# Kernel tuning notes

Hardware: AMD Instinct MI355X
Metric: run time of the kernel (lower is better)

The kernel has to match this reference:

```python
import jax, jax.numpy as jnp
import numpy as np
import math

B, S, D, H = 2, 2048, 1024, 16
HD = D // H


def setup_inputs() -> dict:
    key = jax.random.key(0)
    ks = jax.random.split(key, 8)
    sc = 0.02
    return {
        "x": jax.random.normal(ks[0], (B, S, D), dtype=jnp.float32),
        "y": jax.random.normal(ks[1], (B, S, D), dtype=jnp.float32),
        "W_kv": jax.random.normal(ks[2], (D, 2 * D), dtype=jnp.float32) * sc,
        "b_kv": jnp.zeros((2 * D,), dtype=jnp.float32),
        "W_q": jax.random.normal(ks[3], (D, D), dtype=jnp.float32) * sc,
        "b_q": jnp.zeros((D,), dtype=jnp.float32),
        "W_o": jax.random.normal(ks[4], (D, D), dtype=jnp.float32) * sc,
        "b_o": jnp.zeros((D,), dtype=jnp.float32),
    }


def reference(x, y, W_kv, b_kv, W_q, b_q, W_o, b_o):
    b, s, d = x.shape
    h, hd = H, HD
    # kv projection from x (the "context"), q projection from y
    kv = x @ W_kv + b_kv                     # [b, s, 2d]
    q = y @ W_q + b_q                        # [b, s, d]
    kv = kv.reshape(b, s, h, 2 * hd).transpose(0, 2, 1, 3)  # [b, h, s, 2hd]
    q = q.reshape(b, s, h, hd).transpose(0, 2, 1, 3)        # [b, h, s, hd]
    k, v = kv[..., :hd], kv[..., hd:]
    scaled = jnp.einsum("bhqd,bhkd->bhqk", q, k) / math.sqrt(hd)  # [b,h,s,s]
    attention = jax.nn.softmax(scaled, axis=-1)  # F.softmax defaults to last dim
    values = jnp.einsum("bhqk,bhkd->bhqd", attention, v)  # [b, h, s, hd]
    # Faithful to the original: reshape [b,h,s,hd] -> [b,s,d] WITHOUT
    # transposing heads back (row-major flatten, heads interleaved).
    values = values.reshape(b, s, d)
    return values @ W_o + b_o
```

## Files before the change

### kernel.cpp

```cpp
#include <hip/hip_runtime.h>
#include <hip/hip_bf16.h>


#define S_LEN 2048
#define D_DIM 1024
#define H_NUM 16
#define HD_DIM 64

typedef __attribute__((ext_vector_type(8))) __bf16 bf16x8;
typedef __attribute__((ext_vector_type(4))) float f32x4;

__device__ __forceinline__ unsigned short f2bf(float f) {
    unsigned int v;
    __builtin_memcpy(&v, &f, 4);
    v = v + 0x7fff + ((v >> 16) & 1);
    return (unsigned short)(v >> 16);
}
__device__ __forceinline__ unsigned int pkbf(float a, float b) {
    __hip_bfloat162 h = __float22bfloat162_rn(float2{a, b});
    unsigned int r;
    __builtin_memcpy(&r, &h, 4);
    return r;
}
__device__ __forceinline__ float sani(float v) {
    unsigned int u;
    __builtin_memcpy(&u, &v, 4);
    return ((u >> 23) & 0xFFu) == 0xFFu ? 0.f : v;
}
__device__ __forceinline__ void gll16(const void* g, void* l) {
    __builtin_amdgcn_global_load_lds(
        (const __attribute__((address_space(1))) void*)g,
        (__attribute__((address_space(3))) void*)l, 16, 0, 0);
}

__global__ __launch_bounds__(256) void cvt_bf16(const float* __restrict__ in,
                                                unsigned short* __restrict__ out, int n) {
    int i = (blockIdx.x * 256 + threadIdx.x) * 8;
    if (i < n) {
        float4 a0 = *(const float4*)&in[i];
        float4 a1 = *(const float4*)&in[i + 4];
        uint4 p;
        p.x = pkbf(a0.x, a0.y); p.y = pkbf(a0.z, a0.w);
        p.z = pkbf(a1.x, a1.y); p.w = pkbf(a1.z, a1.w);
        *(uint4*)&out[i] = p;
    }
}

__global__ __launch_bounds__(256) void transpose_cvt(const float* __restrict__ in,
                                                     unsigned short* __restrict__ out,
                                                     int R, int C) {
    __shared__ unsigned short tile[32][33];
    int c0 = blockIdx.x * 32, r0 = blockIdx.y * 32;
    int tx = threadIdx.x & 31, ty = threadIdx.x >> 5;
    for (int i = 0; i < 32; i += 8)
        tile[ty + i][tx] = f2bf(in[(size_t)(r0 + ty + i) * C + c0 + tx]);
    __syncthreads();
    for (int i = 0; i < 32; i += 8)
        out[(size_t)(c0 + ty + i) * R + r0 + tx] = tile[tx][ty + i];
}

template <int AMODE, int CMODE>
__global__ __launch_bounds__(256) void gemm_bt(const void* __restrict__ Av,
                                               const unsigned short* __restrict__ Bt,
                                               const float* __restrict__ bias,
                                               void* __restrict__ C0,
                                               unsigned short* __restrict__ VtB,
                                               int M, int N, int K) {
    constexpr int SA = (AMODE == 1) ? 32 : 40;
    __shared__ unsigned short sA[128 * SA];
    __shared__ unsigned short sB[128 * 32];
    const int tid = threadIdx.x;
    const int m0 = blockIdx.y * 128;
    const int n0 = blockIdx.x * 128;
    const int w = tid >> 6, lane = tid & 63;
    const int quad = lane >> 4, lm = lane & 15;
    const int wrow = (w >> 1) * 64, wcol = (w & 1) * 64;

    f32x4 acc[4][4] = {};

    for (int k0 = 0; k0 < K; k0 += 32) {
        __syncthreads();
#pragma unroll
        for (int p = 0; p < 2; ++p) {
            int cid = p * 256 + tid;
            int row = cid >> 2, col = (cid & 3) << 3;
            if (AMODE == 1) {
                gll16(&((const unsigned short*)Av)[(size_t)(m0 + row) * K + k0 + col],
                      &sA[cid * 8]);
            } else if (AMODE == 0) {
                const float* Af = (const float*)Av + (size_t)(m0 + row) * K + k0 + col;
                float4 a0 = *(const float4*)Af;
                float4 a1 = *(const float4*)(Af + 4);
                uint4 packed;
                packed.x = pkbf(a0.x, a0.y); packed.y = pkbf(a0.z, a0.w);
                packed.z = pkbf(a1.x, a1.y); packed.w = pkbf(a1.z, a1.w);
                *(uint4*)&sA[row * SA + col] = packed;
            } else {
                int m = m0 + row;
                int bb = m >> 11, sib = m & 2047;
                int hh = sib >> 7, qhi = sib & 127;
                int kk = k0 + col;
                uint4 packed = *(const uint4*)((const unsigned short*)Av +
                    (size_t)((bb << 11) + (qhi << 4) + (kk >> 6)) * K + (hh << 6) + (kk & 63));
                *(uint4*)&sA[row * SA + col] = packed;
            }
            gll16(&Bt[(size_t)(n0 + row) * K + k0 + col], &sB[cid * 8]);
        }
        __syncthreads();
        bf16x8 av[4], bv[4];
#pragma unroll
        for (int i = 0; i < 4; ++i)
            av[i] = *(const bf16x8*)&sA[(wrow + i * 16 + lm) * SA + quad * 8];
#pragma unroll
        for (int j = 0; j < 4; ++j)
            bv[j] = *(const bf16x8*)&sB[(wcol + j * 16 + lm) * 32 + quad * 8];
#pragma unroll
        for (int i = 0; i < 4; ++i)
#pragma unroll
            for (int j = 0; j < 4; ++j)
                acc[i][j] = __builtin_amdgcn_mfma_f32_16x16x32_bf16(av[i], bv[j], acc[i][j], 0, 0, 0);
    }

    if (CMODE == 2) {
        const int h = n0 >> 7;
        if (wcol == 0) {
#pragma unroll
            for (int i = 0; i < 4; ++i)
#pragma unroll
                for (int j = 0; j < 4; ++j) {
                    int d = j * 16 + lm;
                    float bi = bias[h * 128 + d];
#pragma unroll
                    for (int r = 0; r < 4; ++r) {
                        int grow = m0 + wrow + i * 16 + quad * 4 + r;
                        int bb = grow >> 11, ss = grow & 2047;
                        ((unsigned short*)C0)[((size_t)(bb * 16 + h) * 2048 + ss) * 64 + d] =
                            f2bf(sani(acc[i][j][r] + bi));
                    }
                }
        } else {
#pragma unroll
            for (int i = 0; i < 4; ++i)
#pragma unroll
                for (int j = 0; j < 4; ++j) {
                    int d = j * 16 + lm;
                    float bi = bias[h * 128 + 64 + d];
                    int s0 = m0 + wrow + i * 16 + quad * 4;
                    int bb = s0 >> 11, ss = s0 & 2047;
                    ushort4 u;
                    u.x = f2bf(sani(acc[i][j][0] + bi));
                    u.y = f2bf(sani(acc[i][j][1] + bi));
                    u.z = f2bf(sani(acc[i][j][2] + bi));
                    u.w = f2bf(sani(acc[i][j][3] + bi));
                    *(ushort4*)&VtB[((size_t)(bb * 16 + h) * 64 + d) * 2048 + ss] = u;
                }
        }
    } else {
#pragma unroll
        for (int i = 0; i < 4; ++i)
#pragma unroll
            for (int j = 0; j < 4; ++j)
#pragma unroll
                for (int r = 0; r < 4; ++r) {
                    int grow = m0 + wrow + i * 16 + quad * 4 + r;
                    int gcol = n0 + wcol + j * 16 + lm;
                    float val = sani(acc[i][j][r] + bias[gcol]);
                    if (CMODE == 1) ((float*)C0)[(size_t)grow * N + gcol] = val;
                    else            ((unsigned short*)C0)[(size_t)grow * N + gcol] = f2bf(val);
                }
    }
}

__global__ __launch_bounds__(256) void attn_k(unsigned short* qo,
                                              const unsigned short* __restrict__ Kb,
                                              const unsigned short* __restrict__ Vt) {
    __shared__ unsigned short sK[64 * 72];
    __shared__ unsigned short sVt[64 * 72];
    __shared__ unsigned short sP[4][16 * 72];

    const int tid = threadIdx.x;
    const int w = tid >> 6, lane = tid & 63;
    const int quad = lane >> 4, lm = lane & 15;
    const int qblock = blockIdx.x & 31;
    const int bh = blockIdx.x >> 5;
    const int b = bh >> 4, h = bh & 15;

    unsigned short* Qp = qo + (size_t)b * S_LEN * D_DIM + h * HD_DIM;
    const unsigned short* Kbase = Kb + (size_t)bh * S_LEN * HD_DIM;
    const unsigned short* Vbase = Vt + (size_t)bh * HD_DIM * S_LEN;

    const int qrow0 = qblock * 64 + w * 16;
    bf16x8 qa0 = *(const bf16x8*)&Qp[(size_t)(qrow0 + lm) * D_DIM + quad * 8];
    bf16x8 qa1 = *(const bf16x8*)&Qp[(size_t)(qrow0 + lm) * D_DIM + 32 + quad * 8];

    f32x4 acc_o[4] = {};
    float lsum[4] = {0.f, 0.f, 0.f, 0.f};

    const int skey = tid >> 2;
    const int sc0 = (tid & 3) * 16;

    for (int kt = 0; kt < S_LEN / 64; ++kt) {
        __syncthreads();
        {
            const unsigned short* Ks = Kbase + (size_t)(kt * 64 + skey) * 64 + sc0;
            *(uint4*)&sK[skey * 72 + sc0]     = *(const uint4*)Ks;
            *(uint4*)&sK[skey * 72 + sc0 + 8] = *(const uint4*)(Ks + 8);
            const unsigned short* Vs = Vbase + (size_t)skey * 2048 + kt * 64 + sc0;
            *(uint4*)&sVt[skey * 72 + sc0]     = *(const uint4*)Vs;
            *(uint4*)&sVt[skey * 72 + sc0 + 8] = *(const uint4*)(Vs + 8);
        }
        __syncthreads();

        unsigned short* sPw = sP[w];
#pragma unroll
        for (int g = 0; g < 4; ++g) {
            bf16x8 k0 = *(const bf16x8*)&sK[(g * 16 + lm) * 72 + quad * 8];
            bf16x8 k1 = *(const bf16x8*)&sK[(g * 16 + lm) * 72 + 32 + quad * 8];
            f32x4 z = {0.f, 0.f, 0.f, 0.f};
            f32x4 c = __builtin_amdgcn_mfma_f32_16x16x32_bf16(
                          qa1, k1,
                          __builtin_amdgcn_mfma_f32_16x16x32_bf16(qa0, k0, z, 0, 0, 0),
                          0, 0, 0);
#pragma unroll
            for (int r = 0; r < 4; ++r) {
                float s = fminf(fmaxf(c[r] * 0.125f, -30.f), 30.f);
                float p = __expf(s);
                lsum[r] += p;
                sPw[(quad * 4 + r) * 72 + g * 16 + lm] = f2bf(p);
            }
        }
        bf16x8 pa0 = *(const bf16x8*)&sPw[lm * 72 + quad * 8];
        bf16x8 pa1 = *(const bf16x8*)&sPw[lm * 72 + 32 + quad * 8];
#pragma unroll
        for (int n = 0; n < 4; ++n) {
            bf16x8 v0 = *(const bf16x8*)&sVt[(n * 16 + lm) * 72 + quad * 8];
            bf16x8 v1 = *(const bf16x8*)&sVt[(n * 16 + lm) * 72 + 32 + quad * 8];
            acc_o[n] = __builtin_amdgcn_mfma_f32_16x16x32_bf16(
                           pa1, v1,
                           __builtin_amdgcn_mfma_f32_16x16x32_bf16(pa0, v0, acc_o[n], 0, 0, 0),
                           0, 0, 0);
        }
    }

#pragma unroll
    for (int r = 0; r < 4; ++r) {
#pragma unroll
        for (int off = 1; off < 16; off <<= 1)
            lsum[r] += __shfl_xor(lsum[r], off);
        float inv = 1.f / lsum[r];
        int qrow = qrow0 + quad * 4 + r;
#pragma unroll
        for (int n = 0; n < 4; ++n)
            Qp[(size_t)qrow * D_DIM + n * 16 + lm] = f2bf(sani(acc_o[n][r] * inv));
    }
}

__global__ __launch_bounds__(256) void fill_k(float* out, int n) {
    int i = blockIdx.x * 256 + threadIdx.x;
    if (i < n) out[i] = 4.0f;
}

extern "C" void kernel_launch(void* const* d_in, const int* in_sizes, int n_in,
                              void* d_out, int out_size, void* d_ws, size_t ws_size,
                              hipStream_t stream) {
    const float* x    = (const float*)d_in[0];
    const float* y    = (const float*)d_in[1];
    const float* W_kv = (const float*)d_in[2];
    const float* b_kv = (const float*)d_in[3];
    const float* W_q  = (const float*)d_in[4];
    const float* b_q  = (const float*)d_in[5];
    const float* W_o  = (const float*)d_in[6];
    const float* b_o  = (const float*)d_in[7];

    if (ws_size < (size_t)16 * 1024 * 1024) {
        fill_k<<<dim3((out_size + 255) / 256), 256, 0, stream>>>((float*)d_out, out_size);
        return;
    }
    const bool bigws = ws_size >= (size_t)26 * 1024 * 1024;

    unsigned short* ws   = (unsigned short*)d_ws;
    unsigned short* Kb   = ws;
    unsigned short* VtB  = ws + 4 * 1024 * 1024;
    unsigned short* xbf  = (unsigned short*)d_out;
    unsigned short* WkvT = xbf + 4 * 1024 * 1024;
    unsigned short* WqT  = WkvT + 2 * 1024 * 1024;
    unsigned short* WoT  = bigws ? ws + 12 * 1024 * 1024
                                 : WqT + 1024 * 1024;
    unsigned short* qBuf = bigws ? ws + 8 * 1024 * 1024
                                 : xbf;
    float* outBuf        = bigws ? (float*)d_out
                                 : (float*)d_ws;

    transpose_cvt<<<dim3(64, 32), 256, 0, stream>>>(W_kv, WkvT, 1024, 2048);
    transpose_cvt<<<dim3(32, 32), 256, 0, stream>>>(W_q, WqT, 1024, 1024);
    transpose_cvt<<<dim3(32, 32), 256, 0, stream>>>(W_o, WoT, 1024, 1024);
    cvt_bf16<<<dim3(2048), 256, 0, stream>>>(x, xbf, 4096 * 1024);
    gemm_bt<1, 2><<<dim3(16, 32), 256, 0, stream>>>(xbf, WkvT, b_kv, Kb, VtB, 4096, 2048, 1024);
    gemm_bt<0, 0><<<dim3(8, 32), 256, 0, stream>>>(y, WqT, b_q, qBuf, nullptr, 4096, 1024, 1024);
    attn_k<<<dim3(2 * H_NUM * (S_LEN / 64)), 256, 0, stream>>>(qBuf, Kb, VtB);
    gemm_bt<2, 1><<<dim3(8, 32), 256, 0, stream>>>(qBuf, WoT, b_o, outBuf, nullptr, 4096, 1024, 1024);
    if (!bigws)
        hipMemcpyAsync(d_out, d_ws, (size_t)out_size * sizeof(float),
                       hipMemcpyDeviceToDevice, stream);
}
```

Before: 279.6 us.

## Merge prep kernels, fuse QKV projections, use async LDS loads in attention

Combines the three weight transposes and the x conversion into one prep launch, and merges the KV and Q projection GEMMs into one grid. The grid is split in two when the workspace is small, because the Q output then aliases xbf. The 1/sqrt(hd) scale moves into the Q projection epilogue and the softmax clamp is removed. Attention now loads K/Vt tiles into LDS with global_load_lds in a split-half layout. The output GEMM uses 64-row tiles to raise the block count. This cuts launch overhead and register round-trips, but removing the clamp risks overflow in exp for large scores.

```diff
diff --git a/kernel.cpp b/kernel.cpp
--- a/kernel.cpp
+++ b/kernel.cpp
@@ -33,84 +33,89 @@
         (__attribute__((address_space(3))) void*)l, 16, 0, 0);
 }
 
-__global__ __launch_bounds__(256) void cvt_bf16(const float* __restrict__ in,
-                                                unsigned short* __restrict__ out, int n) {
-    int i = (blockIdx.x * 256 + threadIdx.x) * 8;
-    if (i < n) {
-        float4 a0 = *(const float4*)&in[i];
-        float4 a1 = *(const float4*)&in[i + 4];
+__global__ __launch_bounds__(256) void prep(const float* __restrict__ Wkv,
+                                            const float* __restrict__ Wq,
+                                            const float* __restrict__ Wo,
+                                            const float* __restrict__ x,
+                                            unsigned short* __restrict__ WkvT,
+                                            unsigned short* __restrict__ WqT,
+                                            unsigned short* __restrict__ WoT,
+                                            unsigned short* __restrict__ xbf) {
+    __shared__ unsigned short tile[32][33];
+    const int blk = blockIdx.x;
+    if (blk < 4096) {
+        const float* in; unsigned short* out; int C, bx, by;
+        if (blk < 2048)      { in = Wkv; out = WkvT; C = 2048; bx = blk & 63;          by = blk >> 6; }
+        else if (blk < 3072) { in = Wq;  out = WqT;  C = 1024; bx = (blk - 2048) & 31; by = (blk - 2048) >> 5; }
+        else                 { in = Wo;  out = WoT;  C = 1024; bx = (blk - 3072) & 31; by = (blk - 3072) >> 5; }
+        const int R = 1024;
+        int c0 = bx * 32, r0 = by * 32;
+        int tx = threadIdx.x & 31, ty = threadIdx.x >> 5;
+        for (int i = 0; i < 32; i += 8)
+            tile[ty + i][tx] = f2bf(in[(size_t)(r0 + ty + i) * C + c0 + tx]);
+        __syncthreads();
+        for (int i = 0; i < 32; i += 8)
+            out[(size_t)(c0 + ty + i) * R + r0 + tx] = tile[tx][ty + i];
+    } else {
+        int i = ((blk - 4096) * 256 + threadIdx.x) * 8;
+        float4 a0 = *(const float4*)&x[i];
+        float4 a1 = *(const float4*)&x[i + 4];
         uint4 p;
         p.x = pkbf(a0.x, a0.y); p.y = pkbf(a0.z, a0.w);
         p.z = pkbf(a1.x, a1.y); p.w = pkbf(a1.z, a1.w);
-        *(uint4*)&out[i] = p;
-    }
-}
-
-__global__ __launch_bounds__(256) void transpose_cvt(const float* __restrict__ in,
-                                                     unsigned short* __restrict__ out,
-                                                     int R, int C) {
-    __shared__ unsigned short tile[32][33];
-    int c0 = blockIdx.x * 32, r0 = blockIdx.y * 32;
-    int tx = threadIdx.x & 31, ty = threadIdx.x >> 5;
-    for (int i = 0; i < 32; i += 8)
-        tile[ty + i][tx] = f2bf(in[(size_t)(r0 + ty + i) * C + c0 + tx]);
-    __syncthreads();
-    for (int i = 0; i < 32; i += 8)
-        out[(size_t)(c0 + ty + i) * R + r0 + tx] = tile[tx][ty + i];
-}
-
-template <int AMODE, int CMODE>
-__global__ __launch_bounds__(256) void gemm_bt(const void* __restrict__ Av,
-                                               const unsigned short* __restrict__ Bt,
-                                               const float* __restrict__ bias,
-                                               void* __restrict__ C0,
-                                               unsigned short* __restrict__ VtB,
-                                               int M, int N, int K) {
-    constexpr int SA = (AMODE == 1) ? 32 : 40;
-    __shared__ unsigned short sA[128 * SA];
+        *(uint4*)&xbf[i] = p;
+    }
+}
+
+__global__ __launch_bounds__(256) void proj(const unsigned short* __restrict__ xbf,
+                                            const float* __restrict__ y,
+                                            const unsigned short* __restrict__ WkvT,
+                                            const unsigned short* __restrict__ WqT,
+                                            const float* __restrict__ b_kv,
+                                            const float* __restrict__ b_q,
+                                            unsigned short* __restrict__ Kb,
+                                            unsigned short* __restrict__ VtB,
+                                            unsigned short* __restrict__ qBuf,
+                                            int base) {
+    __shared__ unsigned short sA[128 * 32];
     __shared__ unsigned short sB[128 * 32];
+    const int blk = blockIdx.x + base;
+    const bool iskv = blk < 512;
+    const int bid = iskv ? blk : blk - 512;
+    const int m0 = iskv ? (bid >> 4) * 128 : (bid >> 3) * 128;
+    const int n0 = iskv ? (bid & 15) * 128 : (bid & 7) * 128;
+    const unsigned short* Bt = iskv ? WkvT : WqT;
     const int tid = threadIdx.x;
-    const int m0 = blockIdx.y * 128;
-    const int n0 = blockIdx.x * 128;
     const int w = tid >> 6, lane = tid & 63;
     const int quad = lane >> 4, lm = lane & 15;
     const int wrow = (w >> 1) * 64, wcol = (w & 1) * 64;
 
     f32x4 acc[4][4] = {};
 
-    for (int k0 = 0; k0 < K; k0 += 32) {
+    for (int k0 = 0; k0 < 1024; k0 += 32) {
         __syncthreads();
 #pragma unroll
         for (int p = 0; p < 2; ++p) {
             int cid = p * 256 + tid;
             int row = cid >> 2, col = (cid & 3) << 3;
-            if (AMODE == 1) {
-                gll16(&((const unsigned short*)Av)[(size_t)(m0 + row) * K + k0 + col],
-                      &sA[cid * 8]);
-            } else if (AMODE == 0) {
-                const float* Af = (const float*)Av + (size_t)(m0 + row) * K + k0 + col;
+            if (iskv) {
+                gll16(&xbf[(size_t)(m0 + row) * 1024 + k0 + col], &sA[cid * 8]);
+            } else {
+                const float* Af = y + (size_t)(m0 + row) * 1024 + k0 + col;
                 float4 a0 = *(const float4*)Af;
                 float4 a1 = *(const float4*)(Af + 4);
-                uint4 packed;
-                packed.x = pkbf(a0.x, a0.y); packed.y = pkbf(a0.z, a0.w);
-                packed.z = pkbf(a1.x, a1.y); packed.w = pkbf(a1.z, a1.w);
-                *(uint4*)&sA[row * SA + col] = packed;
-            } else {
-                int m = m0 + row;
-                int bb = m >> 11, sib = m & 2047;
-                int hh = sib >> 7, qhi = sib & 127;
-                int kk = k0 + col;
-                uint4 packed = *(const uint4*)((const unsigned short*)Av +
-                    (size_t)((bb << 11) + (qhi << 4) + (kk >> 6)) * K + (hh << 6) + (kk & 63));
-                *(uint4*)&sA[row * SA + col] = packed;
+                uint4 pk;
+                pk.x = pkbf(a0.x, a0.y); pk.y = pkbf(a0.z, a0.w);
+                pk.z = pkbf(a1.x, a1.y); pk.w = pkbf(a1.z, a1.w);
+                *(uint4*)&sA[cid * 8] = pk;
             }
-            gll16(&Bt[(size_t)(n0 + row) * K + k0 + col], &sB[cid * 8]);
+            gll16(&Bt[(size_t)(n0 + row) * 1024 + k0 + col], &sB[cid * 8]);
         }
         __syncthreads();
         bf16x8 av[4], bv[4];
 #pragma unroll
         for (int i = 0; i < 4; ++i)
-            av[i] = *(const bf16x8*)&sA[(wrow + i * 16 + lm) * SA + quad * 8];
+            av[i] = *(const bf16x8*)&sA[(wrow + i * 16 + lm) * 32 + quad * 8];
 #pragma unroll
         for (int j = 0; j < 4; ++j)
             bv[j] = *(const bf16x8*)&sB[(wcol + j * 16 + lm) * 32 + quad * 8];
@@ -121,7 +126,7 @@
                 acc[i][j] = __builtin_amdgcn_mfma_f32_16x16x32_bf16(av[i], bv[j], acc[i][j], 0, 0, 0);
     }
 
-    if (CMODE == 2) {
+    if (iskv) {
         const int h = n0 >> 7;
         if (wcol == 0) {
 #pragma unroll
@@ -129,12 +134,12 @@
 #pragma unroll
                 for (int j = 0; j < 4; ++j) {
                     int d = j * 16 + lm;
-                    float bi = bias[h * 128 + d];
+                    float bi = b_kv[h * 128 + d];
 #pragma unroll
                     for (int r = 0; r < 4; ++r) {
                         int grow = m0 + wrow + i * 16 + quad * 4 + r;
                         int bb = grow >> 11, ss = grow & 2047;
-                        ((unsigned short*)C0)[((size_t)(bb * 16 + h) * 2048 + ss) * 64 + d] =
+                        Kb[((size_t)(bb * 16 + h) * 2048 + ss) * 64 + d] =
                             f2bf(sani(acc[i][j][r] + bi));
                     }
                 }
@@ -144,7 +149,7 @@
 #pragma unroll
                 for (int j = 0; j < 4; ++j) {
                     int d = j * 16 + lm;
-                    float bi = bias[h * 128 + 64 + d];
+                    float bi = b_kv[h * 128 + 64 + d];
                     int s0 = m0 + wrow + i * 16 + quad * 4;
                     int bb = s0 >> 11, ss = s0 & 2047;
                     ushort4 u;
@@ -164,9 +169,8 @@
                 for (int r = 0; r < 4; ++r) {
                     int grow = m0 + wrow + i * 16 + quad * 4 + r;
                     int gcol = n0 + wcol + j * 16 + lm;
-                    float val = sani(acc[i][j][r] + bias[gcol]);
-                    if (CMODE == 1) ((float*)C0)[(size_t)grow * N + gcol] = val;
-                    else            ((unsigned short*)C0)[(size_t)grow * N + gcol] = f2bf(val);
+                    float val = sani(acc[i][j][r] + b_q[gcol]) * 0.125f;
+                    qBuf[(size_t)grow * 1024 + gcol] = f2bf(val);
                 }
     }
 }
@@ -174,8 +178,8 @@
 __global__ __launch_bounds__(256) void attn_k(unsigned short* qo,
                                               const unsigned short* __restrict__ Kb,
                                               const unsigned short* __restrict__ Vt) {
-    __shared__ unsigned short sK[64 * 72];
-    __shared__ unsigned short sVt[64 * 72];
+    __shared__ unsigned short sK[2][64 * 32];
+    __shared__ unsigned short sVt[2][64 * 32];
     __shared__ unsigned short sP[4][16 * 72];
 
     const int tid = threadIdx.x;
@@ -196,26 +200,26 @@
     f32x4 acc_o[4] = {};
     float lsum[4] = {0.f, 0.f, 0.f, 0.f};
 
-    const int skey = tid >> 2;
-    const int sc0 = (tid & 3) * 16;
+    const int srow = tid >> 2;
+    const int sch = (tid & 3) << 3;
 
     for (int kt = 0; kt < S_LEN / 64; ++kt) {
         __syncthreads();
         {
-            const unsigned short* Ks = Kbase + (size_t)(kt * 64 + skey) * 64 + sc0;
-            *(uint4*)&sK[skey * 72 + sc0]     = *(const uint4*)Ks;
-            *(uint4*)&sK[skey * 72 + sc0 + 8] = *(const uint4*)(Ks + 8);
-            const unsigned short* Vs = Vbase + (size_t)skey * 2048 + kt * 64 + sc0;
-            *(uint4*)&sVt[skey * 72 + sc0]     = *(const uint4*)Vs;
-            *(uint4*)&sVt[skey * 72 + sc0 + 8] = *(const uint4*)(Vs + 8);
+            const unsigned short* Kr = Kbase + (size_t)(kt * 64 + srow) * 64 + sch;
+            gll16(Kr,      &sK[0][tid * 8]);
+            gll16(Kr + 32, &sK[1][tid * 8]);
+            const unsigned short* Vr = Vbase + (size_t)srow * 2048 + kt * 64 + sch;
+            gll16(Vr,      &sVt[0][tid * 8]);
+            gll16(Vr + 32, &sVt[1][tid * 8]);
         }
         __syncthreads();
 
         unsigned short* sPw = sP[w];
 #pragma unroll
         for (int g = 0; g < 4; ++g) {
-            bf16x8 k0 = *(const bf16x8*)&sK[(g * 16 + lm) * 72 + quad * 8];
-            bf16x8 k1 = *(const bf16x8*)&sK[(g * 16 + lm) * 72 + 32 + quad * 8];
+            bf16x8 k0 = *(const bf16x8*)&sK[0][(g * 16 + lm) * 32 + quad * 8];
+            bf16x8 k1 = *(const bf16x8*)&sK[1][(g * 16 + lm) * 32 + quad * 8];
             f32x4 z = {0.f, 0.f, 0.f, 0.f};
             f32x4 c = __builtin_amdgcn_mfma_f32_16x16x32_bf16(
                           qa1, k1,
@@ -223,8 +227,7 @@
                           0, 0, 0);
 #pragma unroll
             for (int r = 0; r < 4; ++r) {
-                float s = fminf(fmaxf(c[r] * 0.125f, -30.f), 30.f);
-                float p = __expf(s);
+                float p = __expf(c[r]);
                 lsum[r] += p;
                 sPw[(quad * 4 + r) * 72 + g * 16 + lm] = f2bf(p);
             }
@@ -233,8 +236,8 @@
         bf16x8 pa1 = *(const bf16x8*)&sPw[lm * 72 + 32 + quad * 8];
 #pragma unroll
         for (int n = 0; n < 4; ++n) {
-            bf16x8 v0 = *(const bf16x8*)&sVt[(n * 16 + lm) * 72 + quad * 8];
-            bf16x8 v1 = *(const bf16x8*)&sVt[(n * 16 + lm) * 72 + 32 + quad * 8];
+            bf16x8 v0 = *(const bf16x8*)&sVt[0][(n * 16 + lm) * 32 + quad * 8];
+            bf16x8 v1 = *(const bf16x8*)&sVt[1][(n * 16 + lm) * 32 + quad * 8];
             acc_o[n] = __builtin_amdgcn_mfma_f32_16x16x32_bf16(
                            pa1, v1,
                            __builtin_amdgcn_mfma_f32_16x16x32_bf16(pa0, v0, acc_o[n], 0, 0, 0),
@@ -253,6 +256,64 @@
         for (int n = 0; n < 4; ++n)
             Qp[(size_t)qrow * D_DIM + n * 16 + lm] = f2bf(sani(acc_o[n][r] * inv));
     }
+}
+
+__global__ __launch_bounds__(256) void fgemm(const unsigned short* __restrict__ O,
+                                             const unsigned short* __restrict__ WoT,
+                                             const float* __restrict__ b_o,
+                                             float* __restrict__ out) {
+    __shared__ unsigned short sA[64 * 32];
+    __shared__ unsigned short sB[128 * 32];
+    const int tid = threadIdx.x;
+    const int m0 = blockIdx.y * 64;
+    const int n0 = blockIdx.x * 128;
+    const int w = tid >> 6, lane = tid & 63;
+    const int quad = lane >> 4, lm = lane & 15;
+    const int wrow = (w >> 1) * 32, wcol = (w & 1) * 64;
+
+    f32x4 acc[2][4] = {};
+
+    for (int k0 = 0; k0 < 1024; k0 += 32) {
+        __syncthreads();
+        {
+            int row = tid >> 2, kk = k0 + ((tid & 3) << 3);
+            int m = m0 + row;
+            int bb = m >> 11, sib = m & 2047;
+            int hh = sib >> 7, qhi = sib & 127;
+            gll16(&O[(size_t)((bb << 11) + (qhi << 4) + (kk >> 6)) * 1024 + (hh << 6) + (kk & 63)],
+                  &sA[tid * 8]);
+        }
+#pragma unroll
+        for (int p = 0; p < 2; ++p) {
+            int cid = p * 256 + tid;
+            int row = cid >> 2, col = (cid & 3) << 3;
+            gll16(&WoT[(size_t)(n0 + row) * 1024 + k0 + col], &sB[cid * 8]);
+        }
+        __syncthreads();
+        bf16x8 av[2], bv[4];
+#pragma unroll
+        for (int i = 0; i < 2; ++i)
+            av[i] = *(const bf16x8*)&sA[(wrow + i * 16 + lm) * 32 + quad * 8];
+#pragma unroll
+        for (int j = 0; j < 4; ++j)
+            bv[j] = *(const bf16x8*)&sB[(wcol + j * 16 + lm) * 32 + quad * 8];
+#pragma unroll
+        for (int i = 0; i < 2; ++i)
+#pragma unroll
+            for (int j = 0; j < 4; ++j)
+                acc[i][j] = __builtin_amdgcn_mfma_f32_16x16x32_bf16(av[i], bv[j], acc[i][j], 0, 0, 0);
+    }
+
+#pragma unroll
+    for (int i = 0; i < 2; ++i)
+#pragma unroll
+        for (int j = 0; j < 4; ++j)
+#pragma unroll
+            for (int r = 0; r < 4; ++r) {
+                int grow = m0 + wrow + i * 16 + quad * 4 + r;
+                int gcol = n0 + wcol + j * 16 + lm;
+                out[(size_t)grow * 1024 + gcol] = sani(acc[i][j][r] + b_o[gcol]);
+            }
 }
 
 __global__ __launch_bounds__(256) void fill_k(float* out, int n) {
@@ -288,17 +349,17 @@
                                  : WqT + 1024 * 1024;
     unsigned short* qBuf = bigws ? ws + 8 * 1024 * 1024
                                  : xbf;
-    float* outBuf        = bigws ? (float*)d_out
-                                 : (float*)d_ws;
-
-    transpose_cvt<<<dim3(64, 32), 256, 0, stream>>>(W_kv, WkvT, 1024, 2048);
-    transpose_cvt<<<dim3(32, 32), 256, 0, stream>>>(W_q, WqT, 1024, 1024);
-    transpose_cvt<<<dim3(32, 32), 256, 0, stream>>>(W_o, WoT, 1024, 1024);
-    cvt_bf16<<<dim3(2048), 256, 0, stream>>>(x, xbf, 4096 * 1024);
-    gemm_bt<1, 2><<<dim3(16, 32), 256, 0, stream>>>(xbf, WkvT, b_kv, Kb, VtB, 4096, 2048, 1024);
-    gemm_bt<0, 0><<<dim3(8, 32), 256, 0, stream>>>(y, WqT, b_q, qBuf, nullptr, 4096, 1024, 1024);
+    float* outBuf        = bigws ? (float*)d_out : (float*)d_ws;
+
+    prep<<<dim3(6144), 256, 0, stream>>>(W_kv, W_q, W_o, x, WkvT, WqT, WoT, xbf);
+    if (bigws) {
+        proj<<<dim3(768), 256, 0, stream>>>(xbf, y, WkvT, WqT, b_kv, b_q, Kb, VtB, qBuf, 0);
+    } else {
+        proj<<<dim3(512), 256, 0, stream>>>(xbf, y, WkvT, WqT, b_kv, b_q, Kb, VtB, qBuf, 0);
+        proj<<<dim3(256), 256, 0, stream>>>(xbf, y, WkvT, WqT, b_kv, b_q, Kb, VtB, qBuf, 512);
+    }
     attn_k<<<dim3(2 * H_NUM * (S_LEN / 64)), 256, 0, stream>>>(qBuf, Kb, VtB);
-    gemm_bt<2, 1><<<dim3(8, 32), 256, 0, stream>>>(qBuf, WoT, b_o, outBuf, nullptr, 4096, 1024, 1024);
+    fgemm<<<dim3(8, 64), 256, 0, stream>>>(qBuf, WoT, b_o, outBuf);
     if (!bigws)
         hipMemcpyAsync(d_out, d_ws, (size_t)out_size * sizeof(float),
                        hipMemcpyDeviceToDevice, stream);
```

Measured after the change: 263.8 us. 1.06x faster.
